# Performance work log

Hardware: AMD Instinct MI355X
Metric: run time of the kernel (lower is better)

## Reference

```python
import jax, jax.numpy as jnp
import numpy as np

DEGREE = 4
NUM_CHARTS = 8
N = 16384
IN_DIM = 29  # 3*(2*4+1) + 2 procedural params


def positional_encoding(x, degree=DEGREE):
    # Faithful to torch order: [x, sin(2^1 pi x), cos(2^1 pi x), ..., sin(2^d pi x), cos(2^d pi x)]
    pe = [x]
    for d in range(1, degree + 1):
        s = (2.0 ** d) * np.pi
        pe.append(jnp.sin(s * x))
        pe.append(jnp.cos(s * x))
    return jnp.concatenate(pe, axis=-1)


def setup_inputs() -> dict:
    key = jax.random.key(0)
    ks = jax.random.split(key, 9)
    h = 256
    sc = 0.05
    return {
        "x": jax.random.normal(ks[0], (N, 3), jnp.float32),
        "proc": jax.random.normal(ks[1], (1, 2), jnp.float32),
        "W0": jax.random.normal(ks[2], (NUM_CHARTS, IN_DIM, h), jnp.float32) * sc,
        "b0": jax.random.normal(ks[3], (NUM_CHARTS, h), jnp.float32) * sc,
        "Wh": jax.random.normal(ks[4], (NUM_CHARTS, 6, h, h), jnp.float32) * sc,
        "bh": jax.random.normal(ks[5], (NUM_CHARTS, 6, h), jnp.float32) * sc,
        "Wl": jax.random.normal(ks[6], (NUM_CHARTS, h, 2), jnp.float32) * sc,
        "bl": jax.random.normal(ks[7], (NUM_CHARTS, 2), jnp.float32) * sc,
        "mlp_idx": jax.random.randint(ks[8], (N,), 0, NUM_CHARTS, jnp.int32),
    }


def reference(x, proc, W0, b0, Wh, bh, Wl, bl, mlp_idx):
    xp = positional_encoding(x)                      # (N, 27)
    proc_rep = jnp.broadcast_to(proc, (xp.shape[0], proc.shape[1]))
    xp = jnp.concatenate([xp, proc_rep], axis=-1)    # (N, 29)

    out = jnp.zeros((xp.shape[0], Wl.shape[-1]), xp.dtype)
    n_hidden = Wh.shape[1]
    for c in range(NUM_CHARTS):                      # small fixed chart loop
        h = jax.nn.relu(xp @ W0[c] + b0[c])          # (N, 256)
        for l in range(n_hidden):
            h = jax.nn.relu(h @ Wh[c, l] + bh[c, l])
        oc = jax.nn.sigmoid(h @ Wl[c] + bl[c])       # (N, 2)
        out = jnp.where((mlp_idx == c)[:, None], oc, out)
    return out
```

## Files before the change

### kernel.cpp

```cpp
#include <hip/hip_runtime.h>
#include <hip/hip_bf16.h>
#include <math.h>

#define NPTS   16384
#define NCH    8
#define MT     64
#define LSTR   264
#define SEG    16384
#define PSEG   2048

typedef short bf16x8 __attribute__((ext_vector_type(8)));
typedef float f32x4  __attribute__((ext_vector_type(4)));

__device__ __forceinline__ float bf2f(unsigned short u){
  union { unsigned int i; float f; } v; v.i = ((unsigned int)u) << 16; return v.f;
}
__device__ __forceinline__ unsigned short f2bf(float f){
  union { float f; unsigned int i; } v; v.f = f;
  unsigned int x = v.i;
  return (unsigned short)((x + 0x7fffu + ((x >> 16) & 1u)) >> 16);
}


__global__ __launch_bounds__(256) void prep_k(
    const float* __restrict__ Wh, const float* __restrict__ W0,
    const int* __restrict__ midx,
    unsigned short* __restrict__ Wth, unsigned short* __restrict__ Wt0,
    int* __restrict__ segcnt, int* __restrict__ bucket){
  int bid = blockIdx.x, tid = threadIdx.x;
  if (bid < 192){
    __shared__ __align__(16) unsigned short tile[64 * LSTR];
    int mat = bid >> 2, ck = bid & 3;
    const float* src = Wh + (size_t)mat * 65536 + (size_t)ck * 64 * 256;
    int r = tid >> 2, seg = (tid & 3) * 64;
    const float* sp = &src[r * 256 + seg];
    #pragma unroll
    for (int j8 = 0; j8 < 8; j8++){
      float4 f0 = *(const float4*)&sp[j8 * 8];
      float4 f1 = *(const float4*)&sp[j8 * 8 + 4];
      __align__(16) unsigned short t8[8];
      t8[0]=f2bf(f0.x); t8[1]=f2bf(f0.y); t8[2]=f2bf(f0.z); t8[3]=f2bf(f0.w);
      t8[4]=f2bf(f1.x); t8[5]=f2bf(f1.y); t8[6]=f2bf(f1.z); t8[7]=f2bf(f1.w);
      *(uint4*)&tile[r * LSTR + seg + j8 * 8] = *(const uint4*)t8;
    }
    __syncthreads();
    unsigned short* dst = Wth + (size_t)mat * 65536 + (size_t)ck * 16384;
    #pragma unroll
    for (int it = 0; it < 8; it++){
      int s = it * 256 + tid;
      int k8l = s >> 8, n = s & 255;
      __align__(16) unsigned short t8[8];
      #pragma unroll
      for (int j = 0; j < 8; j++) t8[j] = tile[(k8l * 8 + j) * LSTR + n];
      *(uint4*)&dst[(size_t)s * 8] = *(const uint4*)t8;
    }
  } else if (bid < 200){
    int c = bid - 192;
    #pragma unroll
    for (int it = 0; it < 4; it++){
      int s = it * 256 + tid;
      int k8 = s >> 8, n = s & 255;
      __align__(16) unsigned short t8[8];
      #pragma unroll
      for (int j = 0; j < 8; j++){
        int k = k8 * 8 + j;
        t8[j] = (k < 29) ? f2bf(W0[(c * 29 + k) * 256 + n]) : (unsigned short)0;
      }
      *(uint4*)&Wt0[(size_t)c * 8192 + (size_t)s * 8] = *(const uint4*)t8;
    }
  } else {
    __shared__ int cur[NCH];
    int sb = bid - 200;
    int lane = tid & 63;
    if (tid < NCH) cur[tid] = 0;
    __syncthreads();
    for (int it = 0; it < 8; it++){
      int i = sb * PSEG + it * 256 + tid;
      int c = midx[i];
      #pragma unroll
      for (int cc = 0; cc < NCH; cc++){
        unsigned long long m = __ballot(c == cc);
        if (!m) continue;
        int leader = (int)(__ffsll((long long)m) - 1);
        int wb = 0;
        if (lane == leader) wb = atomicAdd(&cur[cc], (int)__popcll(m));
        wb = __shfl(wb, leader);
        if (c == cc){
          int rk = (int)__popcll(m & ((1ull << lane) - 1));
          bucket[cc * SEG + sb * PSEG + wb + rk] = i;
        }
      }
    }
    __syncthreads();
    if (tid < NCH) segcnt[sb * NCH + tid] = cur[tid];
  }
}


__global__ __launch_bounds__(256, 1) void mlp_k(
    const float* __restrict__ x,
    const float* __restrict__ proc,
    const float* __restrict__ b0,
    const float* __restrict__ bh,
    const float* __restrict__ Wl,
    const float* __restrict__ bl,
    const unsigned short* __restrict__ Wt0,
    const unsigned short* __restrict__ Wth,
    const int* __restrict__ segcnt,
    const int* __restrict__ bucket,
    float* __restrict__ out)
{
  __shared__ __align__(16) unsigned short actA[MT * LSTR];
  __shared__ __align__(16) unsigned short actB[MT * LSTR];
  __shared__ float biasb[7 * 256];
  __shared__ float wlb[512];
  __shared__ int ridx[MT];

  int chart = blockIdx.x & 7;
  int tile  = blockIdx.x >> 3;

  int pre[9];
  pre[0] = 0;
  #pragma unroll
  for (int s = 0; s < 8; s++) pre[s + 1] = pre[s] + segcnt[s * NCH + chart];
  int total = pre[8];
  int cnt = total - tile * MT;
  if (cnt <= 0) return;
  if (cnt > MT) cnt = MT;

  int tid  = threadIdx.x;
  int lane = tid & 63;
  int wv   = tid >> 6;
  int l15  = lane & 15;
  int quad = lane >> 4;
  int cb   = wv * 64;

  biasb[tid] = b0[chart * 256 + tid];
  #pragma unroll
  for (int j = 0; j < 6; j++)
    biasb[(j + 1) * 256 + tid] = bh[(chart * 6 + j) * 256 + tid];
  wlb[tid]       = Wl[chart * 512 + tid];
  wlb[256 + tid] = Wl[chart * 512 + 256 + tid];

  if (tid < MT){
    int row = tid;
    int g = -1;
    if (row < cnt){
      int r = tile * MT + row;
      int sb = 0, off = 0;
      #pragma unroll
      for (int s = 0; s < 8; s++)
        if (r >= pre[s]){ sb = s; off = r - pre[s]; }
      g = bucket[chart * SEG + sb * PSEG + off];
    }
    ridx[row] = g;
    unsigned short* rowp = &actA[row * LSTR];
    if (g >= 0){
      float xv0 = x[g*3+0], xv1 = x[g*3+1], xv2 = x[g*3+2];
      rowp[0] = f2bf(xv0); rowp[1] = f2bf(xv1); rowp[2] = f2bf(xv2);
      #pragma unroll
      for (int d = 1; d <= 4; d++){
        float s = (float)(1 << d) * 3.14159265358979323846f;
        int o = 3 + (d - 1) * 6;
        rowp[o+0] = f2bf(sinf(s*xv0)); rowp[o+1] = f2bf(sinf(s*xv1)); rowp[o+2] = f2bf(sinf(s*xv2));
        rowp[o+3] = f2bf(cosf(s*xv0)); rowp[o+4] = f2bf(cosf(s*xv1)); rowp[o+5] = f2bf(cosf(s*xv2));
      }
      rowp[27] = f2bf(proc[0]); rowp[28] = f2bf(proc[1]);
      rowp[29] = 0; rowp[30] = 0; rowp[31] = 0;
    } else {
      #pragma unroll
      for (int k = 0; k < 32; k++) rowp[k] = 0;
    }
  }
  __syncthreads();

  f32x4 acc[4][4];
  const f32x4 zz = {0.f, 0.f, 0.f, 0.f};

  {
    const unsigned short* W0p = Wt0 + chart * 8192;
    bf16x8 b0r[4];
    #pragma unroll
    for (int nt = 0; nt < 4; nt++)
      b0r[nt] = *(const bf16x8*)&W0p[(size_t)(quad * 256 + cb + nt * 16 + l15) * 8];
    #pragma unroll
    for (int mt = 0; mt < 4; mt++){
      bf16x8 a0 = *(const bf16x8*)&actA[(mt * 16 + l15) * LSTR + quad * 8];
      #pragma unroll
      for (int nt = 0; nt < 4; nt++)
        acc[mt][nt] = __builtin_amdgcn_mfma_f32_16x16x32_bf16(a0, b0r[nt], zz, 0, 0, 0);
    }
    #pragma unroll
    for (int nt = 0; nt < 4; nt++){
      int col = cb + nt * 16 + l15;
      float bias = biasb[col];
      #pragma unroll
      for (int mt = 0; mt < 4; mt++)
        #pragma unroll
        for (int r = 0; r < 4; r++){
          float v = acc[mt][nt][r] + bias;
          v = v > 0.f ? v : 0.f;
          actB[(mt * 16 + quad * 4 + r) * LSTR + col] = f2bf(v);
        }
    }
  }
  __syncthreads();

  for (int l = 1; l <= 6; l++){
    const unsigned short* wl8 = Wth + ((size_t)(chart * 6 + l - 1) << 16);
    const unsigned short* ain = (l & 1) ? actB : actA;
    unsigned short* aout      = (l & 1) ? actA : actB;

    bf16x8 breg[8][4];
    #pragma unroll
    for (int kk = 0; kk < 8; kk++)
      #pragma unroll
      for (int nt = 0; nt < 4; nt++)
        breg[kk][nt] = *(const bf16x8*)
            &wl8[(size_t)((kk * 4 + quad) * 256 + cb + nt * 16 + l15) * 8];

    #pragma unroll
    for (int mt = 0; mt < 4; mt++){
      bf16x8 a[8];
      #pragma unroll
      for (int kk = 0; kk < 8; kk++)
        a[kk] = *(const bf16x8*)&ain[(mt * 16 + l15) * LSTR + kk * 32 + quad * 8];
      #pragma unroll
      for (int kk = 0; kk < 8; kk++)
        #pragma unroll
        for (int nt = 0; nt < 4; nt++)
          acc[mt][nt] = __builtin_amdgcn_mfma_f32_16x16x32_bf16(
              a[kk], breg[kk][nt], (kk == 0) ? zz : acc[mt][nt], 0, 0, 0);
    }

    #pragma unroll
    for (int nt = 0; nt < 4; nt++){
      int col = cb + nt * 16 + l15;
      float bias = biasb[l * 256 + col];
      #pragma unroll
      for (int mt = 0; mt < 4; mt++)
        #pragma unroll
        for (int r = 0; r < 4; r++){
          float v = acc[mt][nt][r] + bias;
          v = v > 0.f ? v : 0.f;
          aout[(mt * 16 + quad * 4 + r) * LSTR + col] = f2bf(v);
        }
    }
    __syncthreads();
  }

  {
    int m = tid >> 2;
    int p = tid & 3;
    const unsigned short* hrow = actB + m * LSTR + p * 64;
    const float* wlp = wlb + p * 128;
    float s0 = 0.f, s1 = 0.f;
    #pragma unroll 8
    for (int k = 0; k < 64; k += 2){
      float4 w4 = *(const float4*)&wlp[k * 2];
      unsigned int h2 = *(const unsigned int*)&hrow[k];
      float hv0 = bf2f((unsigned short)(h2 & 0xffff));
      float hv1 = bf2f((unsigned short)(h2 >> 16));
      s0 += hv0 * w4.x + hv1 * w4.z;
      s1 += hv0 * w4.y + hv1 * w4.w;
    }
    s0 += __shfl_xor(s0, 1); s0 += __shfl_xor(s0, 2);
    s1 += __shfl_xor(s1, 1); s1 += __shfl_xor(s1, 2);
    if (p == 0){
      int g = ridx[m];
      if (g >= 0){
        float o0 = 1.f / (1.f + __expf(-(s0 + bl[chart*2+0])));
        float o1 = 1.f / (1.f + __expf(-(s1 + bl[chart*2+1])));
        *(float2*)&out[(size_t)g * 2] = make_float2(o0, o1);
      }
    }
  }
}


extern "C" void kernel_launch(void* const* d_in, const int* in_sizes, int n_in,
                              void* d_out, int out_size, void* d_ws, size_t ws_size,
                              hipStream_t stream){
  const float* x    = (const float*)d_in[0];
  const float* proc = (const float*)d_in[1];
  const float* W0   = (const float*)d_in[2];
  const float* b0   = (const float*)d_in[3];
  const float* Wh   = (const float*)d_in[4];
  const float* bh   = (const float*)d_in[5];
  const float* Wl   = (const float*)d_in[6];
  const float* bl   = (const float*)d_in[7];
  const int* midx = (const int*)d_in[8];
  float* out = (float*)d_out;

  char* ws = (char*)d_ws;
  int* segcnt = (int*)ws;
  int* bucket = segcnt + 64;
  size_t off = (((size_t)(64 + NCH * SEG)) * 4 + 15) & ~(size_t)15;
  unsigned short* Wt0 = (unsigned short*)(ws + off);
  unsigned short* Wth = Wt0 + NCH * 8192;

  hipLaunchKernelGGL(prep_k, dim3(208),  dim3(256), 0, stream,
                     Wh, W0, midx, Wth, Wt0, segcnt, bucket);
  hipLaunchKernelGGL(mlp_k,  dim3(2048), dim3(256), 0, stream,
                     x, proc, b0, bh, Wl, bl, Wt0, Wth, segcnt, bucket, out);
}
```

Baseline: 128.4 us.

## Double-buffer hidden-layer weight registers and prefetch next layer during MFMA compute

Weights for the first hidden layer and the input layer are issued before the positional-encoding prologue, and each hidden layer prefetches the next layer's weight fragments into a second register set while its own MFMAs run. The barriers are replaced with inline asm that waits only on LDS counters (lgkmcnt), so outstanding global weight loads are not drained at each barrier. This aims to hide global-memory latency for weights behind compute. It doubles weight-register usage (64 bf16x8 vectors), which risks spills or lower occupancy.

```diff
diff --git a/kernel.cpp b/kernel.cpp
--- a/kernel.cpp
+++ b/kernel.cpp
@@ -135,6 +135,25 @@
   int quad = lane >> 4;
   int cb   = wv * 64;
 
+  f32x4 acc[4][4];
+  const f32x4 zz = {0.f, 0.f, 0.f, 0.f};
+  bf16x8 bregA[8][4], bregB[8][4];
+  bf16x8 b0r[4];
+
+  {
+    const unsigned short* W0p = Wt0 + chart * 8192;
+    #pragma unroll
+    for (int nt = 0; nt < 4; nt++)
+      b0r[nt] = *(const bf16x8*)&W0p[(size_t)(quad * 256 + cb + nt * 16 + l15) * 8];
+    const unsigned short* w1 = Wth + ((size_t)(chart * 6) << 16);
+    #pragma unroll
+    for (int kk = 0; kk < 8; kk++)
+      #pragma unroll
+      for (int nt = 0; nt < 4; nt++)
+        bregA[kk][nt] = *(const bf16x8*)
+            &w1[(size_t)((kk * 4 + quad) * 256 + cb + nt * 16 + l15) * 8];
+  }
+
   biasb[tid] = b0[chart * 256 + tid];
   #pragma unroll
   for (int j = 0; j < 6; j++)
@@ -174,15 +193,7 @@
   }
   __syncthreads();
 
-  f32x4 acc[4][4];
-  const f32x4 zz = {0.f, 0.f, 0.f, 0.f};
-
   {
-    const unsigned short* W0p = Wt0 + chart * 8192;
-    bf16x8 b0r[4];
-    #pragma unroll
-    for (int nt = 0; nt < 4; nt++)
-      b0r[nt] = *(const bf16x8*)&W0p[(size_t)(quad * 256 + cb + nt * 16 + l15) * 8];
     #pragma unroll
     for (int mt = 0; mt < 4; mt++){
       bf16x8 a0 = *(const bf16x8*)&actA[(mt * 16 + l15) * LSTR + quad * 8];
@@ -203,51 +214,56 @@
           actB[(mt * 16 + quad * 4 + r) * LSTR + col] = f2bf(v);
         }
     }
-  }
-  __syncthreads();
-
-  for (int l = 1; l <= 6; l++){
-    const unsigned short* wl8 = Wth + ((size_t)(chart * 6 + l - 1) << 16);
-    const unsigned short* ain = (l & 1) ? actB : actA;
-    unsigned short* aout      = (l & 1) ? actA : actB;
-
-    bf16x8 breg[8][4];
-    #pragma unroll
-    for (int kk = 0; kk < 8; kk++)
-      #pragma unroll
-      for (int nt = 0; nt < 4; nt++)
-        breg[kk][nt] = *(const bf16x8*)
-            &wl8[(size_t)((kk * 4 + quad) * 256 + cb + nt * 16 + l15) * 8];
-
-    #pragma unroll
-    for (int mt = 0; mt < 4; mt++){
-      bf16x8 a[8];
-      #pragma unroll
-      for (int kk = 0; kk < 8; kk++)
-        a[kk] = *(const bf16x8*)&ain[(mt * 16 + l15) * LSTR + kk * 32 + quad * 8];
-      #pragma unroll
-      for (int kk = 0; kk < 8; kk++)
-        #pragma unroll
-        for (int nt = 0; nt < 4; nt++)
-          acc[mt][nt] = __builtin_amdgcn_mfma_f32_16x16x32_bf16(
-              a[kk], breg[kk][nt], (kk == 0) ? zz : acc[mt][nt], 0, 0, 0);
-    }
-
-    #pragma unroll
-    for (int nt = 0; nt < 4; nt++){
-      int col = cb + nt * 16 + l15;
-      float bias = biasb[l * 256 + col];
-      #pragma unroll
-      for (int mt = 0; mt < 4; mt++)
-        #pragma unroll
-        for (int r = 0; r < 4; r++){
-          float v = acc[mt][nt][r] + bias;
-          v = v > 0.f ? v : 0.f;
-          aout[(mt * 16 + quad * 4 + r) * LSTR + col] = f2bf(v);
-        }
-    }
-    __syncthreads();
-  }
+    asm volatile("s_waitcnt lgkmcnt(0)\n\ts_barrier" ::: "memory");
+  }
+
+#define LAYER(L, CUR, NXT, AIN, AOUT, PF)                                      \
+  {                                                                            \
+    if (PF){                                                                   \
+      const unsigned short* wn = Wth + ((size_t)(chart * 6 + (L)) << 16);      \
+      _Pragma("unroll")                                                        \
+      for (int kk = 0; kk < 8; kk++)                                           \
+        _Pragma("unroll")                                                      \
+        for (int nt = 0; nt < 4; nt++)                                         \
+          NXT[kk][nt] = *(const bf16x8*)                                       \
+              &wn[(size_t)((kk * 4 + quad) * 256 + cb + nt * 16 + l15) * 8];   \
+    }                                                                          \
+    _Pragma("unroll")                                                          \
+    for (int mt = 0; mt < 4; mt++){                                            \
+      bf16x8 a[8];                                                             \
+      _Pragma("unroll")                                                        \
+      for (int kk = 0; kk < 8; kk++)                                           \
+        a[kk] = *(const bf16x8*)&AIN[(mt * 16 + l15) * LSTR + kk * 32 + quad * 8]; \
+      _Pragma("unroll")                                                        \
+      for (int kk = 0; kk < 8; kk++)                                           \
+        _Pragma("unroll")                                                      \
+        for (int nt = 0; nt < 4; nt++)                                         \
+          acc[mt][nt] = __builtin_amdgcn_mfma_f32_16x16x32_bf16(               \
+              a[kk], CUR[kk][nt], (kk == 0) ? zz : acc[mt][nt], 0, 0, 0);      \
+    }                                                                          \
+    _Pragma("unroll")                                                          \
+    for (int nt = 0; nt < 4; nt++){                                            \
+      int col = cb + nt * 16 + l15;                                            \
+      float bias = biasb[(L) * 256 + col];                                     \
+      _Pragma("unroll")                                                        \
+      for (int mt = 0; mt < 4; mt++)                                           \
+        _Pragma("unroll")                                                      \
+        for (int r = 0; r < 4; r++){                                           \
+          float v = acc[mt][nt][r] + bias;                                     \
+          v = v > 0.f ? v : 0.f;                                               \
+          AOUT[(mt * 16 + quad * 4 + r) * LSTR + col] = f2bf(v);               \
+        }                                                                      \
+    }                                                                          \
+    asm volatile("s_waitcnt lgkmcnt(0)\n\ts_barrier" ::: "memory");            \
+  }
+
+  LAYER(1, bregA, bregB, actB, actA, 1)
+  LAYER(2, bregB, bregA, actA, actB, 1)
+  LAYER(3, bregA, bregB, actB, actA, 1)
+  LAYER(4, bregB, bregA, actA, actB, 1)
+  LAYER(5, bregA, bregB, actB, actA, 1)
+  LAYER(6, bregB, bregA, actA, actB, 0)
+#undef LAYER
 
   {
     int m = tid >> 2;
```

After: 148.0 us. +15.3%, slower.
